# Optimization experiments

Hardware: AMD Instinct MI355X
Metric: run time of the kernel (lower is better)

Reference implementation:

```python
import jax, jax.numpy as jnp
import numpy as np

VB = 1.0
N_COORD = 2
N_WALKERS = 2_000_000


def setup_inputs() -> dict:
    key = jax.random.key(0)
    Rs = jax.random.normal(key, (N_WALKERS, N_COORD, 3), dtype=jnp.float32)
    return {
        "Rs": Rs,
        "a": jnp.ones((1,), dtype=jnp.float32),
        "c100_re": jnp.ones((1,), dtype=jnp.float32),
        "c100_im": jnp.zeros((1,), dtype=jnp.float32),
        "c200_re": jnp.ones((1,), dtype=jnp.float32),
        "c200_im": jnp.zeros((1,), dtype=jnp.float32),
    }


def reference(Rs, a, c100_re, c100_im, c200_re, c200_im):
    # Rs: [N, 2, 3] walker coordinates for 2 particles.
    Z = 1.0 / a[0]
    r = jnp.sqrt(jnp.sum(Rs * Rs, axis=-1))            # [N, 2] radial coords
    Y00 = 1.0 / jnp.sqrt(4.0 * jnp.float32(np.pi))     # spherical harmonic Y_00

    # hydrogen-like s-orbitals: psi_100, psi_200 (per particle)
    psi100 = (2.0 * Z ** 1.5 * jnp.exp(-Z * r)) * Y00                       # [N, 2]
    psi200 = (Z ** 1.5 / (2.0 * jnp.sqrt(jnp.float32(2.0)))
              * (2.0 - Z * r) * jnp.exp(-0.5 * Z * r)) * Y00                # [N, 2]

    # product wavefunctions over the two coordinates
    Psi1 = jnp.prod(psi100, axis=-1)   # [N]
    Psi2 = jnp.prod(psi200, axis=-1)   # [N]

    # Laplacian of s-orbital product: sum_a (Z^2/n^2 - 2Z/r_a) * Psi
    inv_r = 1.0 / r
    lap1 = jnp.sum(Z * Z - 2.0 * Z * inv_r, axis=-1)          # [N], n=1
    lap2 = jnp.sum(0.25 * Z * Z - 2.0 * Z * inv_r, axis=-1)   # [N], n=2

    # pairwise Coulomb potential (single pair for N_coord=2)
    d12 = jnp.sqrt(jnp.sum((Rs[:, 0, :] - Rs[:, 1, :]) ** 2, axis=-1))  # [N]
    V = -VB / d12

    H1 = -0.5 * lap1 * Psi1 + V * Psi1   # [N]
    H2 = -0.5 * lap2 * Psi2 + V * Psi2   # [N]

    c1 = (c100_re[0] + 1j * c100_im[0]).astype(jnp.complex64)
    c2 = (c200_re[0] + 1j * c200_im[0]).astype(jnp.complex64)

    H_psi = c1 * H1 + c2 * H2                         # [N] complex64
    psi = c1 * Psi1 + c2 * Psi2                       # [N] complex64
    psistar = jnp.conj(c1) * Psi1 + jnp.conj(c2) * Psi2  # Psi1/Psi2 are real

    hammy = psistar * H_psi
    psi2 = psistar * psi
    return jnp.mean(hammy) / jnp.mean(psi2)
```

## Files before the change

kernel.cpp:

```cpp
#include <hip/hip_runtime.h>
#include <math.h>

#define BLOCK  256
#define GRID   1024
#define NCOMP  7

__device__ __forceinline__ void walker_accum(
    float x0, float y0, float z0, float x1, float y1, float z1,
    float Z, float zz, float ch, float K1, float K2,
    float& a11, float& a22, float& a12, float& a21,
    float& p11, float& p22, float& p12)
{
    float rr0 = x0*x0 + y0*y0 + z0*z0;
    float rr1 = x1*x1 + y1*y1 + z1*z1;
    float q0  = __builtin_amdgcn_rsqf(rr0);
    float q1  = __builtin_amdgcn_rsqf(rr1);
    float r0  = rr0 * q0;
    float r1  = rr1 * q1;

    float h0 = __builtin_amdgcn_exp2f(ch * r0);
    float h1 = __builtin_amdgcn_exp2f(ch * r1);
    float hh = h0 * h1;

    float Psi1 = K1 * (hh * hh);
    float Psi2 = K2 * (2.0f - Z*r0) * (2.0f - Z*r1) * hh;

    float sinv = q0 + q1;

    float dx = x0 - x1, dy = y0 - y1, dz = z0 - z1;
    float dd = dx*dx + dy*dy + dz*dz;
    float V  = -__builtin_amdgcn_rsqf(dd);

    float t1 = Z * sinv - zz + V;
    float t2 = Z * sinv - 0.25f * zz + V;
    float H1 = t1 * Psi1;
    float H2 = t2 * Psi2;

    a11 += Psi1 * H1;
    a22 += Psi2 * H2;
    a12 += Psi1 * H2;
    a21 += Psi2 * H1;
    p11 += Psi1 * Psi1;
    p22 += Psi2 * Psi2;
    p12 += Psi1 * Psi2;
}

__global__ __launch_bounds__(BLOCK) void wvfn_partial(
    const float4* __restrict__ Rs4,
    const float* __restrict__ a_p,
    double* __restrict__ partials,
    int npairs)
{
    const float Z  = 1.0f / a_p[0];
    const float zz = Z * Z;
    const float ch = -0.5f * Z * 1.4426950408889634f;
    const float Y00sq = 0.07957747154594767f;
    const float Z3 = Z * zz;
    const float K1 = 4.0f * Z3 * Y00sq;
    const float K2 = 0.125f * Z3 * Y00sq;

    float a11 = 0.f, a22 = 0.f, a12 = 0.f, a21 = 0.f;
    float p11 = 0.f, p22 = 0.f, p12 = 0.f;

    const int tid    = blockIdx.x * BLOCK + threadIdx.x;
    const int stride = GRID * BLOCK;
    for (int j = tid; j < npairs; j += stride) {
        float4 v0 = Rs4[3*j + 0];
        float4 v1 = Rs4[3*j + 1];
        float4 v2 = Rs4[3*j + 2];
        walker_accum(v0.x, v0.y, v0.z, v0.w, v1.x, v1.y,
                     Z, zz, ch, K1, K2, a11, a22, a12, a21, p11, p22, p12);
        walker_accum(v1.z, v1.w, v2.x, v2.y, v2.z, v2.w,
                     Z, zz, ch, K1, K2, a11, a22, a12, a21, p11, p22, p12);
    }

    double s[NCOMP] = { (double)a11, (double)a22, (double)a12, (double)a21,
                        (double)p11, (double)p22, (double)p12 };

    for (int off = 32; off > 0; off >>= 1) {
        #pragma unroll
        for (int c = 0; c < NCOMP; ++c) s[c] += __shfl_down(s[c], off);
    }

    __shared__ double sm[NCOMP][BLOCK / 64];
    int wid  = threadIdx.x >> 6;
    int lane = threadIdx.x & 63;
    if (lane == 0) {
        #pragma unroll
        for (int c = 0; c < NCOMP; ++c) sm[c][wid] = s[c];
    }
    __syncthreads();
    if (threadIdx.x == 0) {
        #pragma unroll
        for (int c = 0; c < NCOMP; ++c) {
            double t = 0.0;
            for (int w = 0; w < BLOCK / 64; ++w) t += sm[c][w];
            partials[c * GRID + blockIdx.x] = t;
        }
    }
}

__global__ __launch_bounds__(BLOCK) void wvfn_finish(
    const double* __restrict__ partials,
    const float* __restrict__ c1r_p, const float* __restrict__ c1i_p,
    const float* __restrict__ c2r_p, const float* __restrict__ c2i_p,
    float* __restrict__ out, int out_size)
{
    double s[NCOMP];
    #pragma unroll
    for (int c = 0; c < NCOMP; ++c) s[c] = 0.0;
    for (int b = threadIdx.x; b < GRID; b += BLOCK) {
        #pragma unroll
        for (int c = 0; c < NCOMP; ++c) s[c] += partials[c * GRID + b];
    }
    for (int off = 32; off > 0; off >>= 1) {
        #pragma unroll
        for (int c = 0; c < NCOMP; ++c) s[c] += __shfl_down(s[c], off);
    }
    __shared__ double sm[NCOMP][BLOCK / 64];
    int wid  = threadIdx.x >> 6;
    int lane = threadIdx.x & 63;
    if (lane == 0) {
        #pragma unroll
        for (int c = 0; c < NCOMP; ++c) sm[c][wid] = s[c];
    }
    __syncthreads();
    if (threadIdx.x == 0) {
        double A11 = 0, A22 = 0, A12 = 0, A21 = 0, P11 = 0, P22 = 0, P12 = 0;
        for (int w = 0; w < BLOCK / 64; ++w) {
            A11 += sm[0][w]; A22 += sm[1][w]; A12 += sm[2][w]; A21 += sm[3][w];
            P11 += sm[4][w]; P22 += sm[5][w]; P12 += sm[6][w];
        }
        double c1r = (double)c1r_p[0], c1i = (double)c1i_p[0];
        double c2r = (double)c2r_p[0], c2i = (double)c2i_p[0];
        double m1 = c1r*c1r + c1i*c1i;
        double m2 = c2r*c2r + c2i*c2i;
        double u  = c1r*c2r + c1i*c2i;
        double v  = c1r*c2i - c1i*c2r;

        double Hre = m1*A11 + m2*A22 + u*(A12 + A21);
        double Him = v*(A12 - A21);
        double Den = m1*P11 + m2*P22 + 2.0*u*P12;

        out[0] = (float)(Hre / Den);
        if (out_size > 1) out[1] = (float)(Him / Den);
    }
}

extern "C" void kernel_launch(void* const* d_in, const int* in_sizes, int n_in,
                              void* d_out, int out_size, void* d_ws, size_t ws_size,
                              hipStream_t stream) {
    const float4* Rs4 = (const float4*)d_in[0];
    const float* a_p  = (const float*)d_in[1];
    const float* c1r  = (const float*)d_in[2];
    const float* c1i  = (const float*)d_in[3];
    const float* c2r  = (const float*)d_in[4];
    const float* c2i  = (const float*)d_in[5];

    int N      = in_sizes[0] / 6;
    int npairs = N / 2;

    double* partials = (double*)d_ws;

    wvfn_partial<<<GRID, BLOCK, 0, stream>>>(Rs4, a_p, partials, npairs);
    wvfn_finish<<<1, BLOCK, 0, stream>>>(partials, c1r, c1i, c2r, c2i,
                                         (float*)d_out, out_size);
}
```

Baseline: 21.89 us.

## Fuse partial and finish kernels via last-block atomic counter reduction

Merges the two-kernel reduction into one kernel. Each block writes its partials with agent-scope atomic stores, then bumps a global counter, and the last block to arrive does the final reduction and the complex ratio. This removes the second kernel launch and its dependency gap, but adds a hipMemsetAsync before each launch to reset the counter, which is itself an extra stream operation. Ordering relies on relaxed atomics plus an explicit vmcnt wait rather than a release/acquire fence.

```diff
diff --git a/kernel.cpp b/kernel.cpp
--- a/kernel.cpp
+++ b/kernel.cpp
@@ -45,11 +45,14 @@
     p12 += Psi1 * Psi2;
 }
 
-__global__ __launch_bounds__(BLOCK) void wvfn_partial(
+__global__ __launch_bounds__(BLOCK) void wvfn_onepass(
     const float4* __restrict__ Rs4,
     const float* __restrict__ a_p,
+    const float* __restrict__ c1r_p, const float* __restrict__ c1i_p,
+    const float* __restrict__ c2r_p, const float* __restrict__ c2i_p,
     double* __restrict__ partials,
-    int npairs)
+    unsigned int* __restrict__ counter,
+    float* __restrict__ out, int out_size, int npairs)
 {
     const float Z  = 1.0f / a_p[0];
     const float zz = Z * Z;
@@ -83,6 +86,7 @@
     }
 
     __shared__ double sm[NCOMP][BLOCK / 64];
+    __shared__ bool isLast;
     int wid  = threadIdx.x >> 6;
     int lane = threadIdx.x & 63;
     if (lane == 0) {
@@ -95,34 +99,34 @@
         for (int c = 0; c < NCOMP; ++c) {
             double t = 0.0;
             for (int w = 0; w < BLOCK / 64; ++w) t += sm[c][w];
-            partials[c * GRID + blockIdx.x] = t;
+            __hip_atomic_store(&partials[c * GRID + blockIdx.x], t,
+                               __ATOMIC_RELAXED, __HIP_MEMORY_SCOPE_AGENT);
         }
+        asm volatile("s_waitcnt vmcnt(0)" ::: "memory");
+        unsigned int prev = __hip_atomic_fetch_add(
+            counter, 1u, __ATOMIC_RELAXED, __HIP_MEMORY_SCOPE_AGENT);
+        isLast = (prev == (unsigned int)(GRID - 1));
     }
-}
+    __syncthreads();
 
-__global__ __launch_bounds__(BLOCK) void wvfn_finish(
-    const double* __restrict__ partials,
-    const float* __restrict__ c1r_p, const float* __restrict__ c1i_p,
-    const float* __restrict__ c2r_p, const float* __restrict__ c2i_p,
-    float* __restrict__ out, int out_size)
-{
-    double s[NCOMP];
+    if (!isLast) return;
+
+    double u[NCOMP];
     #pragma unroll
-    for (int c = 0; c < NCOMP; ++c) s[c] = 0.0;
+    for (int c = 0; c < NCOMP; ++c) u[c] = 0.0;
     for (int b = threadIdx.x; b < GRID; b += BLOCK) {
         #pragma unroll
-        for (int c = 0; c < NCOMP; ++c) s[c] += partials[c * GRID + b];
+        for (int c = 0; c < NCOMP; ++c)
+            u[c] += __hip_atomic_load(&partials[c * GRID + b],
+                                      __ATOMIC_RELAXED, __HIP_MEMORY_SCOPE_AGENT);
     }
     for (int off = 32; off > 0; off >>= 1) {
         #pragma unroll
-        for (int c = 0; c < NCOMP; ++c) s[c] += __shfl_down(s[c], off);
+        for (int c = 0; c < NCOMP; ++c) u[c] += __shfl_down(u[c], off);
     }
-    __shared__ double sm[NCOMP][BLOCK / 64];
-    int wid  = threadIdx.x >> 6;
-    int lane = threadIdx.x & 63;
     if (lane == 0) {
         #pragma unroll
-        for (int c = 0; c < NCOMP; ++c) sm[c][wid] = s[c];
+        for (int c = 0; c < NCOMP; ++c) sm[c][wid] = u[c];
     }
     __syncthreads();
     if (threadIdx.x == 0) {
@@ -135,12 +139,12 @@
         double c2r = (double)c2r_p[0], c2i = (double)c2i_p[0];
         double m1 = c1r*c1r + c1i*c1i;
         double m2 = c2r*c2r + c2i*c2i;
-        double u  = c1r*c2r + c1i*c2i;
-        double v  = c1r*c2i - c1i*c2r;
+        double uu = c1r*c2r + c1i*c2i;
+        double vv = c1r*c2i - c1i*c2r;
 
-        double Hre = m1*A11 + m2*A22 + u*(A12 + A21);
-        double Him = v*(A12 - A21);
-        double Den = m1*P11 + m2*P22 + 2.0*u*P12;
+        double Hre = m1*A11 + m2*A22 + uu*(A12 + A21);
+        double Him = vv*(A12 - A21);
+        double Den = m1*P11 + m2*P22 + 2.0*uu*P12;
 
         out[0] = (float)(Hre / Den);
         if (out_size > 1) out[1] = (float)(Him / Den);
@@ -160,9 +164,12 @@
     int N      = in_sizes[0] / 6;
     int npairs = N / 2;
 
-    double* partials = (double*)d_ws;
+    unsigned int* counter  = (unsigned int*)d_ws;
+    double*       partials = (double*)((char*)d_ws + 16);
 
-    wvfn_partial<<<GRID, BLOCK, 0, stream>>>(Rs4, a_p, partials, npairs);
-    wvfn_finish<<<1, BLOCK, 0, stream>>>(partials, c1r, c1i, c2r, c2i,
-                                         (float*)d_out, out_size);
+    hipMemsetAsync(counter, 0, sizeof(unsigned int), stream);
+
+    wvfn_onepass<<<GRID, BLOCK, 0, stream>>>(Rs4, a_p, c1r, c1i, c2r, c2i,
+                                             partials, counter,
+                                             (float*)d_out, out_size, npairs);
 }
```

After: 32.67 us. 1.49x slower.
